# Kernel optimization log

Measured on AMD Instinct MI355X. Metric: run time of the kernel, lower is better.

The kernel has to match this reference:

```python
import jax, jax.numpy as jnp
import numpy as np

VOX = 64      # vox_size
KS = 21       # smooth_ks (odd -> 'SAME' == pad ks//2)
SIGMA = 3.0   # smooth_sigma


def smoothing_kernel():
    # normalized 1D gaussian used separably along the 3 voxel axes
    x = jnp.arange(KS, dtype=jnp.float32) - (KS - 1) / 2.0
    g = jnp.exp(-(x * x) / (2.0 * SIGMA * SIGMA))
    return g / g.sum()


def pc_voxels(pc, size):
    """Trilinear scatter of points in [-0.5,0.5]^3 into a [B,size,size,size] grid."""
    B, N, _ = pc.shape
    g = (pc + 0.5) * (size - 1)            # grid coords
    fl = jnp.floor(g)
    idx = fl.astype(jnp.int32)             # [B,N,3] lower corner
    frac = g - fl                          # trilinear fractions
    # 8 corner offsets in {0,1}^3
    offs = jnp.array([[(i >> 2) & 1, (i >> 1) & 1, i & 1] for i in range(8)], dtype=jnp.int32)
    pos = idx[:, :, None, :] + offs[None, None]                       # [B,N,8,3]
    w = jnp.prod(jnp.where(offs[None, None].astype(bool),
                           frac[:, :, None, :], 1.0 - frac[:, :, None, :]), axis=-1)  # [B,N,8]
    inb = jnp.all((pos >= 0) & (pos < size), axis=-1)
    w = jnp.where(inb, w, 0.0)
    posc = jnp.clip(pos, 0, size - 1)
    # voxel layout vox[b, z, y, x]; pc columns are (x, y, z)
    flat = posc[..., 2] * (size * size) + posc[..., 1] * size + posc[..., 0]
    vox = jnp.zeros((B, size * size * size), pc.dtype)
    vox = vox.at[jnp.arange(B)[:, None, None], flat].add(w)
    return jnp.clip(vox.reshape(B, size, size, size), 0.0, 1.0)


def voxels_smooth(v, g1d, scale):
    """Separable 3D Gaussian smoothing + per-batch scale, clamped to [0,1]."""
    x = v[:, None]  # NCDHW, C=1
    ks = g1d.shape[0]
    for kshape in ((1, 1, ks, 1, 1), (1, 1, 1, ks, 1), (1, 1, 1, 1, ks)):
        x = jax.lax.conv_general_dilated(
            x, g1d.reshape(kshape), (1, 1, 1), 'SAME',
            dimension_numbers=('NCDHW', 'OIDHW', 'NCDHW'))
    x = x[:, 0] * scale[:, None, None, None]
    return jnp.clip(x, 0.0, 1.0)


def drc_prob(v):
    """DRC ray-termination probabilities along depth (axis 1)."""
    trans = jnp.cumprod(1.0 - v, axis=1)                                   # [B,D,H,W]
    tshift = jnp.concatenate([jnp.ones_like(trans[:, :1]), trans[:, :-1]], axis=1)
    stop = v * tshift                                                      # stop at voxel d
    esc = trans[:, -1:]                                                    # ray escapes
    return jnp.concatenate([stop, esc], axis=1)                            # [B,D+1,H,W]


def reference(pc, rotation, scale):
    pc_t = jnp.einsum('bni,bji->bnj', pc, rotation)   # camera transform: pc @ R^T
    vox = pc_voxels(pc_t, VOX)
    sm = voxels_smooth(vox, smoothing_kernel(), scale)
    prob = drc_prob(sm)
    proj = prob[:, :-1].sum(1)[:, ::-1, :]            # sum over depth, flip rows
    return proj


def setup_inputs() -> dict:
    key = jax.random.key(0)
    k1, k2, k3 = jax.random.split(key, 3)
    B, N = 32, 65536
    pc = jax.random.uniform(k1, (B, N, 3), jnp.float32) - 0.5   # points in [-0.5, 0.5]
    q, _ = jnp.linalg.qr(jax.random.normal(k2, (B, 3, 3), jnp.float32))  # random rotations
    scale = 0.5 + jax.random.uniform(k3, (B,), jnp.float32)
    return {"pc": pc, "rotation": q, "scale": scale}
```

## Files before the change

kernel.cpp:

```cpp
#include <hip/hip_runtime.h>

#define NB    32
#define NP    65536
#define SZ    64
#define SZ3   (SZ * SZ * SZ)
#define KS    21
#define HALF  10
#define NBIN4 260
#define CAP4  1024
#define FXS   960.0f

typedef _Float16 half8_t __attribute__((ext_vector_type(8)));
typedef _Float16 half4_t __attribute__((ext_vector_type(4)));
typedef float    f32x4_t __attribute__((ext_vector_type(4)));

__device__ __forceinline__ int swz(int row, int col) {
    return (row << 6) + ((((col >> 3) ^ (row & 7))) << 3) + (col & 7);
}

__device__ __forceinline__ void weights_reg(float* w) {
    float sum = 0.0f;
#pragma unroll
    for (int k = 0; k < KS; ++k) {
        float d = (float)k - (float)HALF;
        w[k] = expf(-d * d / 18.0f);
        sum += w[k];
    }
#pragma unroll
    for (int k = 0; k < KS; ++k) w[k] /= sum;
}

__device__ __forceinline__ void fma4(float4& a, float t, const float4& v) {
    a.x = fmaf(t, v.x, a.x); a.y = fmaf(t, v.y, a.y);
    a.z = fmaf(t, v.z, a.z); a.w = fmaf(t, v.w, a.w);
}

__device__ __forceinline__ unsigned pack_fx(float g) {
    float c = fminf(fmaxf(g, -2.0f), 65.0f);
    return (unsigned)__float2uint_rn((c + 2.0f) * FXS);
}

__global__ void fill_kernel(const float* __restrict__ pc,
                            const float* __restrict__ rot,
                            int* __restrict__ cur,
                            uint2* __restrict__ binned,
                            _Float16* __restrict__ Gg) {
    __shared__ int h[4][NBIN4];
    __shared__ int woff[4][NBIN4];
    __shared__ int lbase[NBIN4];
    int base = blockIdx.x * 1024;
    int b = base >> 16;
    int wv = threadIdx.x >> 6;
    for (int i = threadIdx.x; i < 4 * NBIN4; i += 256) h[i / NBIN4][i % NBIN4] = 0;
    __syncthreads();
    const float* R = rot + b * 9;
    const float4* p4 = (const float4*)(pc + (size_t)base * 3);
    float4 f0 = p4[threadIdx.x * 3 + 0];
    float4 f1 = p4[threadIdx.x * 3 + 1];
    float4 f2 = p4[threadIdx.x * 3 + 2];
    float px[4] = {f0.x, f0.w, f1.z, f2.y};
    float py[4] = {f0.y, f1.x, f1.w, f2.z};
    float pz[4] = {f0.z, f1.y, f2.x, f2.w};
    uint2 pk[4];
    int bn[4][4], lp[4][4];
#pragma unroll
    for (int j = 0; j < 4; ++j) {
        float g0 = (R[0] * px[j] + R[1] * py[j] + R[2] * pz[j] + 0.5f) * 63.0f;
        float g1 = (R[3] * px[j] + R[4] * py[j] + R[5] * pz[j] + 0.5f) * 63.0f;
        float g2 = (R[6] * px[j] + R[7] * py[j] + R[8] * pz[j] + 0.5f) * 63.0f;
        int i2 = (int)floorf(g2);
        int i1 = (int)floorf(g1);
        int i0 = (int)floorf(g0);
        bool zv = (i2 >= -1 && i2 <= 63);
        int h0 = ((unsigned)i1       < 64u) ? (i1 >> 5)       : -1;
        int h1 = ((unsigned)(i1 + 1) < 64u) ? ((i1 + 1) >> 5) : -1;
        if (h1 == h0) h1 = -1;
        int v0 = ((unsigned)i0       < 64u) ? (i0 >> 5)       : -1;
        int v1 = ((unsigned)(i0 + 1) < 64u) ? ((i0 + 1) >> 5) : -1;
        if (v1 == v0) v1 = -1;
        int zb = (i2 + 1) * 2;
        bn[j][0] = (zv && h0 >= 0 && v0 >= 0) ? ((zb + h0) * 2 + v0) : -1;
        bn[j][1] = (zv && h0 >= 0 && v1 >= 0) ? ((zb + h0) * 2 + v1) : -1;
        bn[j][2] = (zv && h1 >= 0 && v0 >= 0) ? ((zb + h1) * 2 + v0) : -1;
        bn[j][3] = (zv && h1 >= 0 && v1 >= 0) ? ((zb + h1) * 2 + v1) : -1;
        pk[j] = make_uint2(pack_fx(g0) | (pack_fx(g1) << 16), pack_fx(g2));
#pragma unroll
        for (int t = 0; t < 4; ++t)
            if (bn[j][t] >= 0) lp[j][t] = atomicAdd(&h[wv][bn[j][t]], 1);
    }
    __syncthreads();
    for (int t = threadIdx.x; t < NBIN4; t += 256) {
        int s0 = h[0][t], s1 = h[1][t], s2 = h[2][t], s3 = h[3][t];
        int tot = s0 + s1 + s2 + s3;
        lbase[t] = tot ? atomicAdd(&cur[b * NBIN4 + t], tot) : 0;
        woff[0][t] = 0; woff[1][t] = s0; woff[2][t] = s0 + s1; woff[3][t] = s0 + s1 + s2;
    }
    __syncthreads();
#pragma unroll
    for (int j = 0; j < 4; ++j) {
#pragma unroll
        for (int t = 0; t < 4; ++t) {
            if (bn[j][t] >= 0) {
                int pos = lbase[bn[j][t]] + woff[wv][bn[j][t]] + lp[j][t];
                if (pos < CAP4)
                    binned[(size_t)(b * NBIN4 + bn[j][t]) * CAP4 + pos] = pk[j];
            }
        }
    }
    if (blockIdx.x == 0) {
        float w[KS];
        weights_reg(w);
        for (int i = threadIdx.x; i < 4096; i += 256) {
            int d = (i >> 6) - (i & 63) + HALF;
            Gg[i] = ((unsigned)d < (unsigned)KS) ? (_Float16)w[d] : (_Float16)0.0f;
        }
    }
}

__global__ void __launch_bounds__(256, 4) splat_blur(const uint2* __restrict__ binned,
                                                     const int* __restrict__ cur,
                                                     const _Float16* __restrict__ Gg,
                                                     _Float16* __restrict__ vox) {
    __shared__ __align__(16) char smem[33792];
    int tid = threadIdx.x;
    int w = tid >> 6, lane = tid & 63;
    int yh = w >> 1, xh = w & 1;
    int idx = blockIdx.x;
    int b = idx >> 6;
    int k = (idx + (b << 3)) & 63;
    int z = (k & 1) ? (31 - (k >> 1)) : (32 + (k >> 1));
    int q = lane >> 4, c = lane & 15;

    _Float16* Ay = (_Float16*)(smem + w * 4224);
    _Float16* Bx = (_Float16*)(smem + 16896 + w * 4224);
    _Float16* P  = (_Float16*)smem;
    _Float16* T  = (_Float16*)(smem + 16896);

    {
        int4 z4 = {0, 0, 0, 0};
        int4* a4 = (int4*)Ay;
        for (int i = lane; i < 4224 / 16; i += 64) a4[i] = z4;
        int4* b4 = (int4*)Bx;
        for (int i = lane; i < 4224 / 16; i += 64) b4[i] = z4;
    }

    int bin0 = (2 * z + yh) * 2 + xh;
    int bin1 = (2 * (z + 1) + yh) * 2 + xh;
    int c0 = min(cur[b * NBIN4 + bin0], CAP4);
    int c1 = min(cur[b * NBIN4 + bin1], CAP4);
    const uint2* s0 = binned + (size_t)(b * NBIN4 + bin0) * CAP4;
    const uint2* s1 = binned + (size_t)(b * NBIN4 + bin1) * CAP4;
    int n = c0 + c1;

    f32x4_t acc[2][2];
#pragma unroll
    for (int ml = 0; ml < 2; ++ml)
#pragma unroll
        for (int ni = 0; ni < 2; ++ni) acc[ml][ni] = (f32x4_t){0.f, 0.f, 0.f, 0.f};

    int iters = (n + 63) >> 6;
    uint2 nxtA = make_uint2(0u, 0u), nxtB = make_uint2(0u, 0u);
    {
        int i0g = lane;
        if (i0g < n) nxtA = (i0g < c0) ? s0[i0g] : s1[i0g - c0];
        int i1g = 64 + lane;
        if (i1g < n) nxtB = (i1g < c0) ? s0[i1g] : s1[i1g - c0];
    }
    for (int it = 0; it < iters; ++it) {
        uint2 pk = nxtA;
        nxtA = nxtB;
        nxtB = make_uint2(0u, 0u);
        int ni2 = (it + 2) * 64 + lane;
        if (ni2 < n) nxtB = (ni2 < c0) ? s0[ni2] : s1[ni2 - c0];

        float gx = (float)(pk.x & 0xffffu) * (1.0f / FXS) - 2.0f;
        float gy = (float)(pk.x >> 16)     * (1.0f / FXS) - 2.0f;
        float gz = (float)(pk.y & 0xffffu) * (1.0f / FXS) - 2.0f;
        float f0 = floorf(gx), f1 = floorf(gy);
        int   i0 = (int)f0,    i1 = (int)f1;
        float r0 = gx - f0,    r1f = gy - f1;
        float az = fmaxf(0.0f, 1.0f - fabsf(gz - (float)z));
        int rlo = i1 - (yh << 5), rhi = rlo + 1;
        int alo = ((unsigned)rlo < 32u) ? rlo : 32;
        int ahi = ((unsigned)rhi < 32u) ? rhi : 32;
        int xg  = i0 - (xh << 5);
        int xlo = ((unsigned)xg       < 32u) ? xg       : 32;
        int xhi = ((unsigned)(xg + 1) < 32u) ? (xg + 1) : 32;
        Ay[swz(alo, lane)] = (_Float16)(az * (1.0f - r1f));
        Ay[swz(ahi, lane)] = (_Float16)(az * r1f);
        Bx[swz(xlo, lane)] = (_Float16)(1.0f - r0);
        Bx[swz(xhi, lane)] = (_Float16)r0;
#pragma unroll
        for (int hh = 0; hh < 2; ++hh) {
            half8_t af[2], bf[2];
#pragma unroll
            for (int ml = 0; ml < 2; ++ml)
                af[ml] = *(const half8_t*)&Ay[swz(ml * 16 + c, hh * 32 + q * 8)];
#pragma unroll
            for (int ni = 0; ni < 2; ++ni)
                bf[ni] = *(const half8_t*)&Bx[swz(ni * 16 + c, hh * 32 + q * 8)];
#pragma unroll
            for (int ml = 0; ml < 2; ++ml)
#pragma unroll
                for (int ni = 0; ni < 2; ++ni)
                    acc[ml][ni] = __builtin_amdgcn_mfma_f32_16x16x32_f16(
                        af[ml], bf[ni], acc[ml][ni], 0, 0, 0);
        }
        Ay[swz(alo, lane)] = (_Float16)0.0f;
        Ay[swz(ahi, lane)] = (_Float16)0.0f;
        Bx[swz(xlo, lane)] = (_Float16)0.0f;
        Bx[swz(xhi, lane)] = (_Float16)0.0f;
    }

    __syncthreads();

    half8_t gf[4][2];
#pragma unroll
    for (int ni = 0; ni < 4; ++ni)
#pragma unroll
        for (int hh = 0; hh < 2; ++hh)
            gf[ni][hh] = *(const half8_t*)&Gg[(ni * 16 + c) * 64 + hh * 32 + q * 8];

#pragma unroll
    for (int ml = 0; ml < 2; ++ml)
#pragma unroll
        for (int ni = 0; ni < 2; ++ni)
#pragma unroll
            for (int r = 0; r < 4; ++r)
                P[swz((yh << 5) + ml * 16 + q * 4 + r, (xh << 5) + ni * 16 + c)] =
                    (_Float16)fminf(fmaxf(acc[ml][ni][r], 0.0f), 1.0f);
    __syncthreads();

    f32x4_t a2[4];
#pragma unroll
    for (int ni = 0; ni < 4; ++ni) a2[ni] = (f32x4_t){0.f, 0.f, 0.f, 0.f};
#pragma unroll
    for (int hh = 0; hh < 2; ++hh) {
        half8_t af1 = *(const half8_t*)&P[swz(w * 16 + c, hh * 32 + q * 8)];
#pragma unroll
        for (int ni = 0; ni < 4; ++ni)
            a2[ni] = __builtin_amdgcn_mfma_f32_16x16x32_f16(
                af1, gf[ni][hh], a2[ni], 0, 0, 0);
    }
#pragma unroll
    for (int ni = 0; ni < 4; ++ni) {
        half4_t pkd;
#pragma unroll
        for (int r = 0; r < 4; ++r) pkd[r] = (_Float16)a2[ni][r];
        *(half4_t*)&T[swz(ni * 16 + c, w * 16 + q * 4)] = pkd;
    }
    __syncthreads();

    f32x4_t a3[4];
#pragma unroll
    for (int ni = 0; ni < 4; ++ni) a3[ni] = (f32x4_t){0.f, 0.f, 0.f, 0.f};
#pragma unroll
    for (int hh = 0; hh < 2; ++hh) {
        half8_t bf1[4];
#pragma unroll
        for (int ni = 0; ni < 4; ++ni)
            bf1[ni] = *(const half8_t*)&T[swz(ni * 16 + c, hh * 32 + q * 8)];
#pragma unroll
        for (int ni = 0; ni < 4; ++ni)
            a3[ni] = __builtin_amdgcn_mfma_f32_16x16x32_f16(
                gf[w][hh], bf1[ni], a3[ni], 0, 0, 0);
    }

    _Float16* dst = vox + ((size_t)b << 18) + ((size_t)z << 12);
#pragma unroll
    for (int ni = 0; ni < 4; ++ni)
#pragma unroll
        for (int r = 0; r < 4; ++r)
            dst[((w * 16 + q * 4 + r) << 6) + ni * 16 + c] = (_Float16)a3[ni][r];
}

__global__ void convz_drc_kernel(const _Float16* __restrict__ in,
                                 const float* __restrict__ scale,
                                 float* __restrict__ out) {
    __shared__ float sraw[640 + SZ * SZ + 640];
    __shared__ float c[SZ * SZ];
    __shared__ float segS[4][64], segT[4][64];
    float* s = sraw + 640;
    int b = blockIdx.x >> 6, y = blockIdx.x & 63;

    for (int i = threadIdx.x; i < 640; i += 256) {
        sraw[i] = 0.0f;
        sraw[640 + SZ * SZ + i] = 0.0f;
    }
    const _Float16* base = in + ((size_t)b << 18) + (y << 6);
#pragma unroll
    for (int g = 0; g < 4; ++g) {
        int cell = g * 256 + threadIdx.x;
        int z = cell >> 4, xc = (cell & 15) << 2;
        half4_t v = *(const half4_t*)&base[((size_t)z << 12) + xc];
        float4 f = make_float4((float)v[0], (float)v[1], (float)v[2], (float)v[3]);
        *(float4*)&s[(z << 6) + xc] = f;
    }
    __syncthreads();

    float w[KS];
    weights_reg(w);

    {
        int z0 = (threadIdx.x >> 4) << 2;
        int xc = (threadIdx.x & 15) << 2;
        float4 a0 = {0,0,0,0}, a1 = {0,0,0,0}, a2 = {0,0,0,0}, a3 = {0,0,0,0};
#pragma unroll
        for (int d = 0; d < 24; ++d) {
            int zz = z0 - HALF + d;
            float4 v = *(const float4*)&s[(zz << 6) + xc];
            if (d <= 20)           fma4(a0, w[d],     v);
            if (d >= 1 && d <= 21) fma4(a1, w[d - 1], v);
            if (d >= 2 && d <= 22) fma4(a2, w[d - 2], v);
            if (d >= 3)            fma4(a3, w[d - 3], v);
        }
        *(float4*)&c[((z0 + 0) << 6) + xc] = a0;
        *(float4*)&c[((z0 + 1) << 6) + xc] = a1;
        *(float4*)&c[((z0 + 2) << 6) + xc] = a2;
        *(float4*)&c[((z0 + 3) << 6) + xc] = a3;
    }
    __syncthreads();

    {
        int x = threadIdx.x & 63, seg = threadIdx.x >> 6;
        float sc = scale[b];
        float trans = 1.0f, sum = 0.0f;
#pragma unroll
        for (int zz = 0; zz < 16; ++zz) {
            int z = seg * 16 + zz;
            float v = fminf(fmaxf(c[(z << 6) + x] * sc, 0.0f), 1.0f);
            sum += v * trans;
            trans *= 1.0f - v;
        }
        segS[seg][x] = sum;
        segT[seg][x] = trans;
    }
    __syncthreads();
    if (threadIdx.x < 64) {
        int x = threadIdx.x;
        float t = 1.0f, S = 0.0f;
#pragma unroll
        for (int sgi = 0; sgi < 4; ++sgi) { S += segS[sgi][x] * t; t *= segT[sgi][x]; }
        out[(b << 12) + ((63 - y) << 6) + x] = S;
    }
}

extern "C" void kernel_launch(void* const* d_in, const int* in_sizes, int n_in,
                              void* d_out, int out_size, void* d_ws, size_t ws_size,
                              hipStream_t stream) {
    const float* pc    = (const float*)d_in[0];
    const float* rot   = (const float*)d_in[1];
    const float* scale = (const float*)d_in[2];
    float* out = (float*)d_out;

    _Float16* vox    = (_Float16*)d_ws;
    uint2*    binned = (uint2*)((char*)d_ws + (size_t)NB * SZ3 * sizeof(_Float16));
    _Float16* Gg     = (_Float16*)((char*)binned + (size_t)NB * NBIN4 * CAP4 * sizeof(uint2));
    int*      cur    = (int*)((char*)Gg + 64 * 64 * sizeof(_Float16));

    hipMemsetAsync(cur, 0, NB * NBIN4 * sizeof(int), stream);

    fill_kernel     <<<NB * NP / 1024, 256, 0, stream>>>(pc, rot, cur, binned, Gg);
    splat_blur      <<<NB * SZ, 256, 0, stream>>>(binned, cur, Gg, vox);
    convz_drc_kernel<<<NB * SZ, 256, 0, stream>>>(vox, scale, out);
}
```

Baseline: 137.0 us.

## Replace MFMA outer-product splat with LDS float atomics and z-only binning

```diff
diff --git a/kernel.cpp b/kernel.cpp
--- a/kernel.cpp
+++ b/kernel.cpp
@@ -6,9 +6,10 @@
 #define SZ3   (SZ * SZ * SZ)
 #define KS    21
 #define HALF  10
-#define NBIN4 260
-#define CAP4  1024
-#define FXS   960.0f
+#define NBINZ 65
+#define CAPZ  2048
+#define PL_W  72
+#define PL_WORDS (70 * PL_W)
 
 typedef _Float16 half8_t __attribute__((ext_vector_type(8)));
 typedef _Float16 half4_t __attribute__((ext_vector_type(4)));
@@ -35,9 +36,12 @@
     a.z = fmaf(t, v.z, a.z); a.w = fmaf(t, v.w, a.w);
 }
 
-__device__ __forceinline__ unsigned pack_fx(float g) {
-    float c = fminf(fmaxf(g, -2.0f), 65.0f);
-    return (unsigned)__float2uint_rn((c + 2.0f) * FXS);
+__device__ __forceinline__ unsigned short h16(float x) {
+    _Float16 h = (_Float16)x;
+    return __builtin_bit_cast(unsigned short, h);
+}
+__device__ __forceinline__ float f16f(unsigned v) {
+    return (float)__builtin_bit_cast(_Float16, (unsigned short)(v & 0xffffu));
 }
 
 __global__ void fill_kernel(const float* __restrict__ pc,
@@ -45,66 +49,54 @@
                             int* __restrict__ cur,
                             uint2* __restrict__ binned,
                             _Float16* __restrict__ Gg) {
-    __shared__ int h[4][NBIN4];
-    __shared__ int woff[4][NBIN4];
-    __shared__ int lbase[NBIN4];
+    __shared__ int h[4][NBINZ];
+    __shared__ int woff[4][NBINZ];
+    __shared__ int lbase[NBINZ];
     int base = blockIdx.x * 1024;
     int b = base >> 16;
     int wv = threadIdx.x >> 6;
-    for (int i = threadIdx.x; i < 4 * NBIN4; i += 256) h[i / NBIN4][i % NBIN4] = 0;
+    for (int i = threadIdx.x; i < 4 * NBINZ; i += 256) h[i / NBINZ][i % NBINZ] = 0;
     __syncthreads();
     const float* R = rot + b * 9;
     const float4* p4 = (const float4*)(pc + (size_t)base * 3);
-    float4 f0 = p4[threadIdx.x * 3 + 0];
-    float4 f1 = p4[threadIdx.x * 3 + 1];
-    float4 f2 = p4[threadIdx.x * 3 + 2];
-    float px[4] = {f0.x, f0.w, f1.z, f2.y};
-    float py[4] = {f0.y, f1.x, f1.w, f2.z};
-    float pz[4] = {f0.z, f1.y, f2.x, f2.w};
+    float4 f0v = p4[threadIdx.x * 3 + 0];
+    float4 f1v = p4[threadIdx.x * 3 + 1];
+    float4 f2v = p4[threadIdx.x * 3 + 2];
+    float px[4] = {f0v.x, f0v.w, f1v.z, f2v.y};
+    float py[4] = {f0v.y, f1v.x, f1v.w, f2v.z};
+    float pz[4] = {f0v.z, f1v.y, f2v.x, f2v.w};
     uint2 pk[4];
-    int bn[4][4], lp[4][4];
+    int bn[4], lp[4];
 #pragma unroll
     for (int j = 0; j < 4; ++j) {
         float g0 = (R[0] * px[j] + R[1] * py[j] + R[2] * pz[j] + 0.5f) * 63.0f;
         float g1 = (R[3] * px[j] + R[4] * py[j] + R[5] * pz[j] + 0.5f) * 63.0f;
         float g2 = (R[6] * px[j] + R[7] * py[j] + R[8] * pz[j] + 0.5f) * 63.0f;
-        int i2 = (int)floorf(g2);
-        int i1 = (int)floorf(g1);
-        int i0 = (int)floorf(g0);
-        bool zv = (i2 >= -1 && i2 <= 63);
-        int h0 = ((unsigned)i1       < 64u) ? (i1 >> 5)       : -1;
-        int h1 = ((unsigned)(i1 + 1) < 64u) ? ((i1 + 1) >> 5) : -1;
-        if (h1 == h0) h1 = -1;
-        int v0 = ((unsigned)i0       < 64u) ? (i0 >> 5)       : -1;
-        int v1 = ((unsigned)(i0 + 1) < 64u) ? ((i0 + 1) >> 5) : -1;
-        if (v1 == v0) v1 = -1;
-        int zb = (i2 + 1) * 2;
-        bn[j][0] = (zv && h0 >= 0 && v0 >= 0) ? ((zb + h0) * 2 + v0) : -1;
-        bn[j][1] = (zv && h0 >= 0 && v1 >= 0) ? ((zb + h0) * 2 + v1) : -1;
-        bn[j][2] = (zv && h1 >= 0 && v0 >= 0) ? ((zb + h1) * 2 + v0) : -1;
-        bn[j][3] = (zv && h1 >= 0 && v1 >= 0) ? ((zb + h1) * 2 + v1) : -1;
-        pk[j] = make_uint2(pack_fx(g0) | (pack_fx(g1) << 16), pack_fx(g2));
-#pragma unroll
-        for (int t = 0; t < 4; ++t)
-            if (bn[j][t] >= 0) lp[j][t] = atomicAdd(&h[wv][bn[j][t]], 1);
-    }
-    __syncthreads();
-    for (int t = threadIdx.x; t < NBIN4; t += 256) {
+        float fl0 = floorf(g0), fl1 = floorf(g1), fl2 = floorf(g2);
+        int i2 = (int)fl2;
+        int i0c = min(max((int)fl0, -2), 65);
+        int i1c = min(max((int)fl1, -2), 65);
+        pk[j].x = (unsigned)(i0c + 2) | ((unsigned)(i1c + 2) << 8)
+                | ((unsigned)h16(g0 - fl0) << 16);
+        pk[j].y = (unsigned)h16(g1 - fl1) | ((unsigned)h16(g2 - fl2) << 16);
+        bn[j] = (i2 >= -1 && i2 <= 63) ? (i2 + 1) : -1;
+        if (bn[j] >= 0) lp[j] = atomicAdd(&h[wv][bn[j]], 1);
+    }
+    __syncthreads();
+    if (threadIdx.x < NBINZ) {
+        int t = threadIdx.x;
         int s0 = h[0][t], s1 = h[1][t], s2 = h[2][t], s3 = h[3][t];
         int tot = s0 + s1 + s2 + s3;
-        lbase[t] = tot ? atomicAdd(&cur[b * NBIN4 + t], tot) : 0;
+        lbase[t] = tot ? atomicAdd(&cur[b * NBINZ + t], tot) : 0;
         woff[0][t] = 0; woff[1][t] = s0; woff[2][t] = s0 + s1; woff[3][t] = s0 + s1 + s2;
     }
     __syncthreads();
 #pragma unroll
     for (int j = 0; j < 4; ++j) {
-#pragma unroll
-        for (int t = 0; t < 4; ++t) {
-            if (bn[j][t] >= 0) {
-                int pos = lbase[bn[j][t]] + woff[wv][bn[j][t]] + lp[j][t];
-                if (pos < CAP4)
-                    binned[(size_t)(b * NBIN4 + bn[j][t]) * CAP4 + pos] = pk[j];
-            }
+        if (bn[j] >= 0) {
+            int pos = lbase[bn[j]] + woff[wv][bn[j]] + lp[j];
+            if (pos < CAPZ)
+                binned[(size_t)(b * NBINZ + bn[j]) * CAPZ + pos] = pk[j];
         }
     }
     if (blockIdx.x == 0) {
@@ -117,101 +109,69 @@
     }
 }
 
-__global__ void __launch_bounds__(256, 4) splat_blur(const uint2* __restrict__ binned,
+__global__ void __launch_bounds__(256, 5) splat_blur(const uint2* __restrict__ binned,
                                                      const int* __restrict__ cur,
                                                      const _Float16* __restrict__ Gg,
                                                      _Float16* __restrict__ vox) {
-    __shared__ __align__(16) char smem[33792];
+    __shared__ __align__(16) char smem[PL_WORDS * 4 + 8192];
+    float*    plane = (float*)smem;
+    _Float16* P     = (_Float16*)(smem + PL_WORDS * 4);
+    _Float16* T     = (_Float16*)smem;
+
     int tid = threadIdx.x;
     int w = tid >> 6, lane = tid & 63;
-    int yh = w >> 1, xh = w & 1;
     int idx = blockIdx.x;
     int b = idx >> 6;
     int k = (idx + (b << 3)) & 63;
     int z = (k & 1) ? (31 - (k >> 1)) : (32 + (k >> 1));
     int q = lane >> 4, c = lane & 15;
 
-    _Float16* Ay = (_Float16*)(smem + w * 4224);
-    _Float16* Bx = (_Float16*)(smem + 16896 + w * 4224);
-    _Float16* P  = (_Float16*)smem;
-    _Float16* T  = (_Float16*)(smem + 16896);
-
     {
         int4 z4 = {0, 0, 0, 0};
-        int4* a4 = (int4*)Ay;
-        for (int i = lane; i < 4224 / 16; i += 64) a4[i] = z4;
-        int4* b4 = (int4*)Bx;
-        for (int i = lane; i < 4224 / 16; i += 64) b4[i] = z4;
-    }
-
-    int bin0 = (2 * z + yh) * 2 + xh;
-    int bin1 = (2 * (z + 1) + yh) * 2 + xh;
-    int c0 = min(cur[b * NBIN4 + bin0], CAP4);
-    int c1 = min(cur[b * NBIN4 + bin1], CAP4);
-    const uint2* s0 = binned + (size_t)(b * NBIN4 + bin0) * CAP4;
-    const uint2* s1 = binned + (size_t)(b * NBIN4 + bin1) * CAP4;
+        int4* p4 = (int4*)plane;
+        for (int i = tid; i < PL_WORDS / 4; i += 256) p4[i] = z4;
+    }
+    __syncthreads();
+
+    int c0 = min(cur[b * NBINZ + z],     CAPZ);
+    int c1 = min(cur[b * NBINZ + z + 1], CAPZ);
     int n = c0 + c1;
-
-    f32x4_t acc[2][2];
-#pragma unroll
-    for (int ml = 0; ml < 2; ++ml)
-#pragma unroll
-        for (int ni = 0; ni < 2; ++ni) acc[ml][ni] = (f32x4_t){0.f, 0.f, 0.f, 0.f};
-
-    int iters = (n + 63) >> 6;
-    uint2 nxtA = make_uint2(0u, 0u), nxtB = make_uint2(0u, 0u);
+    const uint2* s0 = binned + (size_t)(b * NBINZ + z) * CAPZ;
+
+    int iters = (n + 255) >> 8;
+    uint2 pA = make_uint2(0u, 0u), pB = make_uint2(0u, 0u);
+    int fA = 0, fB = 0;
     {
-        int i0g = lane;
-        if (i0g < n) nxtA = (i0g < c0) ? s0[i0g] : s1[i0g - c0];
-        int i1g = 64 + lane;
-        if (i1g < n) nxtB = (i1g < c0) ? s0[i1g] : s1[i1g - c0];
+        int i0g = tid;
+        if (i0g < n) { fA = i0g >= c0; pA = s0[i0g + (fA ? CAPZ - c0 : 0)]; }
+        int i1g = 256 + tid;
+        if (i1g < n) { fB = i1g >= c0; pB = s0[i1g + (fB ? CAPZ - c0 : 0)]; }
     }
     for (int it = 0; it < iters; ++it) {
-        uint2 pk = nxtA;
-        nxtA = nxtB;
-        nxtB = make_uint2(0u, 0u);
-        int ni2 = (it + 2) * 64 + lane;
-        if (ni2 < n) nxtB = (ni2 < c0) ? s0[ni2] : s1[ni2 - c0];
-
-        float gx = (float)(pk.x & 0xffffu) * (1.0f / FXS) - 2.0f;
-        float gy = (float)(pk.x >> 16)     * (1.0f / FXS) - 2.0f;
-        float gz = (float)(pk.y & 0xffffu) * (1.0f / FXS) - 2.0f;
-        float f0 = floorf(gx), f1 = floorf(gy);
-        int   i0 = (int)f0,    i1 = (int)f1;
-        float r0 = gx - f0,    r1f = gy - f1;
-        float az = fmaxf(0.0f, 1.0f - fabsf(gz - (float)z));
-        int rlo = i1 - (yh << 5), rhi = rlo + 1;
-        int alo = ((unsigned)rlo < 32u) ? rlo : 32;
-        int ahi = ((unsigned)rhi < 32u) ? rhi : 32;
-        int xg  = i0 - (xh << 5);
-        int xlo = ((unsigned)xg       < 32u) ? xg       : 32;
-        int xhi = ((unsigned)(xg + 1) < 32u) ? (xg + 1) : 32;
-        Ay[swz(alo, lane)] = (_Float16)(az * (1.0f - r1f));
-        Ay[swz(ahi, lane)] = (_Float16)(az * r1f);
-        Bx[swz(xlo, lane)] = (_Float16)(1.0f - r0);
-        Bx[swz(xhi, lane)] = (_Float16)r0;
-#pragma unroll
-        for (int hh = 0; hh < 2; ++hh) {
-            half8_t af[2], bf[2];
-#pragma unroll
-            for (int ml = 0; ml < 2; ++ml)
-                af[ml] = *(const half8_t*)&Ay[swz(ml * 16 + c, hh * 32 + q * 8)];
-#pragma unroll
-            for (int ni = 0; ni < 2; ++ni)
-                bf[ni] = *(const half8_t*)&Bx[swz(ni * 16 + c, hh * 32 + q * 8)];
-#pragma unroll
-            for (int ml = 0; ml < 2; ++ml)
-#pragma unroll
-                for (int ni = 0; ni < 2; ++ni)
-                    acc[ml][ni] = __builtin_amdgcn_mfma_f32_16x16x32_f16(
-                        af[ml], bf[ni], acc[ml][ni], 0, 0, 0);
-        }
-        Ay[swz(alo, lane)] = (_Float16)0.0f;
-        Ay[swz(ahi, lane)] = (_Float16)0.0f;
-        Bx[swz(xlo, lane)] = (_Float16)0.0f;
-        Bx[swz(xhi, lane)] = (_Float16)0.0f;
-    }
-
+        uint2 pk = pA; int fk = fA;
+        pA = pB; fA = fB;
+        pB = make_uint2(0u, 0u); fB = 0;
+        int ni = (it + 2) * 256 + tid;
+        if (ni < n) { fB = ni >= c0; pB = s0[ni + (fB ? CAPZ - c0 : 0)]; }
+
+        int col = pk.x & 0xff;
+        int row = (pk.x >> 8) & 0xff;
+        float r0 = f16f(pk.x >> 16);
+        float r1 = f16f(pk.y);
+        float fz = f16f(pk.y >> 16);
+        float az  = fk ? 1.0f - fz : fz;
+        float ay1 = az * r1;
+        float ay0 = az - ay1;
+        float w01 = ay0 * r0;
+        float w00 = ay0 - w01;
+        float w11 = ay1 * r0;
+        float w10 = ay1 - w11;
+        float* cell = plane + row * PL_W + col;
+        atomicAdd(cell,            w00);
+        atomicAdd(cell + 1,        w01);
+        atomicAdd(cell + PL_W,     w10);
+        atomicAdd(cell + PL_W + 1, w11);
+    }
     __syncthreads();
 
     half8_t gf[4][2];
@@ -221,14 +181,11 @@
         for (int hh = 0; hh < 2; ++hh)
             gf[ni][hh] = *(const half8_t*)&Gg[(ni * 16 + c) * 64 + hh * 32 + q * 8];
 
-#pragma unroll
-    for (int ml = 0; ml < 2; ++ml)
-#pragma unroll
-        for (int ni = 0; ni < 2; ++ni)
-#pragma unroll
-            for (int r = 0; r < 4; ++r)
-                P[swz((yh << 5) + ml * 16 + q * 4 + r, (xh << 5) + ni * 16 + c)] =
-                    (_Float16)fminf(fmaxf(acc[ml][ni][r], 0.0f), 1.0f);
+    for (int i = tid; i < 4096; i += 256) {
+        int Y = i >> 6, X = i & 63;
+        float v = plane[(Y + 2) * PL_W + (X + 2)];
+        P[swz(Y, X)] = (_Float16)fminf(fmaxf(v, 0.0f), 1.0f);
+    }
     __syncthreads();
 
     f32x4_t a2[4];
@@ -355,10 +312,10 @@
 
     _Float16* vox    = (_Float16*)d_ws;
     uint2*    binned = (uint2*)((char*)d_ws + (size_t)NB * SZ3 * sizeof(_Float16));
-    _Float16* Gg     = (_Float16*)((char*)binned + (size_t)NB * NBIN4 * CAP4 * sizeof(uint2));
+    _Float16* Gg     = (_Float16*)((char*)binned + (size_t)NB * NBINZ * CAPZ * sizeof(uint2));
     int*      cur    = (int*)((char*)Gg + 64 * 64 * sizeof(_Float16));
 
-    hipMemsetAsync(cur, 0, NB * NBIN4 * sizeof(int), stream);
+    hipMemsetAsync(cur, 0, NB * NBINZ * sizeof(int), stream);
 
     fill_kernel     <<<NB * NP / 1024, 256, 0, stream>>>(pc, rot, cur, binned, Gg);
     splat_blur      <<<NB * SZ, 256, 0, stream>>>(binned, cur, Gg, vox);
```

Measured after the change: 203.5 us. 48.5% more time.
